# Kernel optimization log

Hardware: AMD Instinct MI355X
Metric: run time of the kernel (lower is better)

The kernel has to match this reference:

```python
import jax, jax.numpy as jnp
import numpy as np

N_NODES = 50000
N_EDGES = 800000
N_GRAPHS = 8
BN_EPS = 1e-5


def setup_inputs() -> dict:
    key = jax.random.key(0)
    ks = iter(jax.random.split(key, 40))
    d = {}
    d["x"] = jax.random.normal(next(ks), (N_NODES, 3), dtype=jnp.float32)
    d["edge_index"] = jax.random.randint(next(ks), (2, N_EDGES), 0, N_NODES, dtype=jnp.int32)
    d["batch"] = jnp.sort(jax.random.randint(next(ks), (N_NODES,), 0, N_GRAPHS, dtype=jnp.int32))
    conv_in = [3, 64, 128]  # dense concat widths feeding each GCN layer
    for i, cin in enumerate(conv_in):
        d[f"W{i}"] = jax.random.normal(next(ks), (cin, 64), dtype=jnp.float32) * (1.0 / np.sqrt(cin))
        d[f"b{i}"] = jax.random.normal(next(ks), (64,), dtype=jnp.float32) * 0.05
        d[f"g{i}"] = jax.random.uniform(next(ks), (64,), dtype=jnp.float32) + 0.5
        d[f"beta{i}"] = jax.random.normal(next(ks), (64,), dtype=jnp.float32) * 0.05
        d[f"rm{i}"] = jax.random.normal(next(ks), (64,), dtype=jnp.float32) * 0.05
        d[f"rv{i}"] = jax.random.uniform(next(ks), (64,), dtype=jnp.float32) + 0.5
    def lin(k, i, o):
        return (jax.random.normal(k, (i, o), dtype=jnp.float32) * (1.0 / np.sqrt(i)),)
    d["enc_w0"], = lin(next(ks), 256, 128); d["enc_b0"] = jax.random.normal(next(ks), (128,), jnp.float32) * 0.05
    d["enc_w1"], = lin(next(ks), 128, 64); d["enc_b1"] = jax.random.normal(next(ks), (64,), jnp.float32) * 0.05
    d["dec_w0"], = lin(next(ks), 64, 32); d["dec_b0"] = jax.random.normal(next(ks), (32,), jnp.float32) * 0.05
    d["dec_w1"], = lin(next(ks), 32, 1); d["dec_b1"] = jax.random.normal(next(ks), (1,), jnp.float32) * 0.05
    return d


def reference(x, edge_index, batch,
              W0, b0, g0, beta0, rm0, rv0,
              W1, b1, g1, beta1, rm1, rv1,
              W2, b2, g2, beta2, rm2, rv2,
              enc_w0, enc_b0, enc_w1, enc_b1,
              dec_w0, dec_b0, dec_w1, dec_b1):
    N = x.shape[0]
    loops = jnp.arange(N, dtype=edge_index.dtype)
    src = jnp.concatenate([edge_index[0], loops])  # GCNConv adds self loops
    dst = jnp.concatenate([edge_index[1], loops])
    deg = jax.ops.segment_sum(jnp.ones_like(src, dtype=x.dtype), dst, num_segments=N)
    dinv = jnp.where(deg > 0, jax.lax.rsqrt(deg), 0.0)
    coef = (dinv[src] * dinv[dst])[:, None]  # symmetric normalization per edge

    def conv_bn_relu(h, W, b, g, beta, rm, rv):
        hw = h @ W                                    # [N, 64]
        out = jax.ops.segment_sum(hw[src] * coef, dst, num_segments=N) + b
        out = (out - rm) * (g * jax.lax.rsqrt(rv + BN_EPS)) + beta  # BN eval mode
        return jax.nn.relu(out)

    params = [(W0, b0, g0, beta0, rm0, rv0),
              (W1, b1, g1, beta1, rm1, rv1),
              (W2, b2, g2, beta2, rm2, rv2)]
    prev = []
    h = x
    for p in params:  # dense connectivity: concat all previous concat-outputs
        h = conv_bn_relu(h, *p)
        h = jnp.concatenate(prev + [h], axis=1)
        prev.append(h)

    e = jax.nn.relu(jax.nn.relu(h @ enc_w0 + enc_b0) @ enc_w1 + enc_b1)  # [N, 64]
    counts = jax.ops.segment_sum(jnp.ones((N,), x.dtype), batch, num_segments=N_GRAPHS)
    gfeat = jax.ops.segment_sum(e, batch, num_segments=N_GRAPHS) / jnp.maximum(counts, 1.0)[:, None]
    out = jax.nn.relu(gfeat @ dec_w0 + dec_b0) @ dec_w1 + dec_b1  # [G, 1]
    return out[:, 0]  # torch.squeeze(output, 1) since num_classes == 1
```

## Files before the change

kernel.cpp:

```cpp
#include <hip/hip_runtime.h>
#include <hip/hip_fp16.h>

#define NN 50000
#define NE 800000
#define NG 8
#define BN_EPS 1e-5f
#define NBLK ((NN + 255) / 256)
#define NPART 8
#define HLD 192

typedef __attribute__((ext_vector_type(8))) short bf16x8;
typedef __attribute__((ext_vector_type(4))) float f32x4;

static __device__ __forceinline__ unsigned short f2bf(float f) {
    unsigned int u = __float_as_uint(f);
    unsigned int r = (u + 0x7FFFu + ((u >> 16) & 1u)) >> 16;
    return (unsigned short)r;
}
static __device__ __forceinline__ float bf2f(unsigned short h) {
    return __uint_as_float((unsigned int)h << 16);
}


__global__ __launch_bounds__(256) void count_deg(const int4* __restrict__ dst4,
                                                 int* __restrict__ degi) {
    int t = blockIdx.x * 256 + threadIdx.x;
    if (t < NE / 4) {
        int4 d = dst4[t];
        atomicAdd(&degi[d.x], 1);
        atomicAdd(&degi[d.y], 1);
        atomicAdd(&degi[d.z], 1);
        atomicAdd(&degi[d.w], 1);
    }
}

__global__ __launch_bounds__(256) void scan_partial(const int* __restrict__ degi,
                                                    const float* __restrict__ x,
                                                    int* __restrict__ rowptr,
                                                    int* __restrict__ bsum,
                                                    float* __restrict__ dinv,
                                                    float* __restrict__ xs) {
    __shared__ int sh[256];
    const int tid = threadIdx.x;
    const int i = blockIdx.x * 256 + tid;
    int v = (i < NN) ? degi[i] : 0;
    if (i < NN) {
        float di = rsqrtf((float)(v + 1));
        dinv[i] = di;
        xs[i * 3 + 0] = x[i * 3 + 0] * di;
        xs[i * 3 + 1] = x[i * 3 + 1] * di;
        xs[i * 3 + 2] = x[i * 3 + 2] * di;
    }
    sh[tid] = v;
    __syncthreads();
#pragma unroll
    for (int off = 1; off < 256; off <<= 1) {
        int t = (tid >= off) ? sh[tid - off] : 0;
        __syncthreads();
        sh[tid] += t;
        __syncthreads();
    }
    if (i < NN) rowptr[i] = sh[tid] - v;
    if (tid == 255) bsum[blockIdx.x] = sh[255];
}

__global__ __launch_bounds__(256) void scan_bsums(int* __restrict__ bsum) {
    __shared__ int sh[256];
    const int tid = threadIdx.x;
    int v = (tid < NBLK) ? bsum[tid] : 0;
    sh[tid] = v;
    __syncthreads();
#pragma unroll
    for (int off = 1; off < 256; off <<= 1) {
        int t = (tid >= off) ? sh[tid - off] : 0;
        __syncthreads();
        sh[tid] += t;
        __syncthreads();
    }
    if (tid < NBLK) bsum[tid] = sh[tid] - v;
}

__global__ __launch_bounds__(256) void scan_finalize(const int* __restrict__ bsum,
                                                     int* __restrict__ rowptr,
                                                     int* __restrict__ cursor) {
    const int i = blockIdx.x * 256 + threadIdx.x;
    if (i < NN) {
        int r = rowptr[i] + bsum[blockIdx.x];
        rowptr[i] = r;
        cursor[i] = r;
    }
    if (i == 0) rowptr[NN] = NE;
}

__global__ __launch_bounds__(256) void fill_csr(const int* __restrict__ src,
                                                const int* __restrict__ dst,
                                                int* __restrict__ cursor,
                                                unsigned short* __restrict__ esrc16) {
    int e = blockIdx.x * 256 + threadIdx.x;
    if (e < NE) {
        int s = src[e], d = dst[e];
        int p = atomicAdd(&cursor[d], 1);
        esrc16[p] = (unsigned short)s;
    }
}


static __device__ __forceinline__ void pack_one(const float* W, int NOUT, int li,
                                                float v_override, bool use_override,
                                                unsigned short* ph, unsigned short* pl) {
    int j = li & 7;
    int lane = (li >> 3) & 63;
    int rest = li >> 9;
    int NF = NOUT >> 4;
    int f = rest % NF, ks = rest / NF;
    int k = ks * 32 + (lane >> 4) * 8 + j;
    int col = f * 16 + (lane & 15);
    float v = use_override ? v_override : W[k * NOUT + col];
    unsigned short hi = f2bf(v);
    ph[li] = hi;
    pl[li] = f2bf(v - bf2f(hi));
}

__global__ __launch_bounds__(256) void pack_all(
        const float* __restrict__ W1, const float* __restrict__ W2,
        const float* __restrict__ We0, const float* __restrict__ We1,
        unsigned short* __restrict__ Wp1h, unsigned short* __restrict__ Wp1l,
        unsigned short* __restrict__ Wp2h, unsigned short* __restrict__ Wp2l,
        unsigned short* __restrict__ We0h, unsigned short* __restrict__ We0l,
        unsigned short* __restrict__ We1h, unsigned short* __restrict__ We1l,
        float* __restrict__ gfeat_part) {
    int idx = blockIdx.x * 256 + threadIdx.x;
    if (idx < NPART * NG * 64) gfeat_part[idx] = 0.0f;
    if (idx < 4096) {
        pack_one(W1, 64, idx, 0.f, false, Wp1h, Wp1l);
    } else if (idx < 12288) {
        pack_one(W2, 64, idx - 4096, 0.f, false, Wp2h, Wp2l);
    } else if (idx < 36864) {
        int li = idx - 12288;
        int j = li & 7;
        int lane = (li >> 3) & 63;
        int rest = li >> 9;
        int f = rest % 8, ks = rest / 8;
        int k = ks * 32 + (lane >> 4) * 8 + j;
        int col = f * 16 + (lane & 15);
        float v = (k < 64) ? (We0[k * 128 + col] + We0[(k + 64) * 128 + col])
                           : We0[(k + 64) * 128 + col];
        pack_one(nullptr, 128, li, v, true, We0h, We0l);
    } else if (idx < 45056) {
        pack_one(We1, 64, idx - 36864, 0.f, false, We1h, We1l);
    }
}


template<int K>
__global__ __launch_bounds__(256, 2) void mfma_tab(
        const unsigned short* __restrict__ Ahi,
        const unsigned short* __restrict__ Alo, int lda,
        const unsigned short* __restrict__ Bph,
        const unsigned short* __restrict__ Bpl,
        const float* __restrict__ dinv,
        __half* __restrict__ outH) {
    constexpr int KS = K / 32;
    const int wave = threadIdx.x >> 6;
    const int lane = threadIdx.x & 63;
    const int rbase = blockIdx.x * 64 + wave * 16;
    int arow = rbase + (lane & 15);
    if (arow >= NN) arow = NN - 1;
    const int kbase = (lane >> 4) * 8;

    bf16x8 bh[KS][4], bl[KS][4];
#pragma unroll
    for (int ks = 0; ks < KS; ks++)
#pragma unroll
        for (int f = 0; f < 4; f++) {
            bh[ks][f] = *reinterpret_cast<const bf16x8*>(Bph + (size_t)((ks * 4 + f) * 64 + lane) * 8);
            bl[ks][f] = *reinterpret_cast<const bf16x8*>(Bpl + (size_t)((ks * 4 + f) * 64 + lane) * 8);
        }

    const unsigned short* pa_hi = Ahi + (size_t)arow * lda + kbase;
    const unsigned short* pa_lo = Alo + (size_t)arow * lda + kbase;
    bf16x8 ah[KS], al[KS];
#pragma unroll
    for (int ks = 0; ks < KS; ks++) {
        ah[ks] = *reinterpret_cast<const bf16x8*>(pa_hi + ks * 32);
        al[ks] = *reinterpret_cast<const bf16x8*>(pa_lo + ks * 32);
    }

    f32x4 acc[4];
#pragma unroll
    for (int f = 0; f < 4; f++) acc[f] = (f32x4){0.f, 0.f, 0.f, 0.f};

#pragma unroll
    for (int ks = 0; ks < KS; ks++)
#pragma unroll
        for (int f = 0; f < 4; f++) {
            acc[f] = __builtin_amdgcn_mfma_f32_16x16x32_bf16(ah[ks], bh[ks][f], acc[f], 0, 0, 0);
            acc[f] = __builtin_amdgcn_mfma_f32_16x16x32_bf16(ah[ks], bl[ks][f], acc[f], 0, 0, 0);
            acc[f] = __builtin_amdgcn_mfma_f32_16x16x32_bf16(al[ks], bh[ks][f], acc[f], 0, 0, 0);
        }

    const int drow0 = rbase + (lane >> 4) * 4;
    const int dcol = lane & 15;
#pragma unroll
    for (int f = 0; f < 4; f++) {
#pragma unroll
        for (int r = 0; r < 4; r++) {
            int row = drow0 + r;
            if (row < NN)
                outH[(size_t)row * 64 + f * 16 + dcol] = __float2half(acc[f][r] * dinv[row]);
        }
    }
}


__global__ __launch_bounds__(256, 2) void enc_fused(
        const unsigned short* __restrict__ Hhi,
        const unsigned short* __restrict__ Hlo,
        const unsigned short* __restrict__ We0h, const unsigned short* __restrict__ We0l,
        const float* __restrict__ b0,
        const unsigned short* __restrict__ We1h, const unsigned short* __restrict__ We1l,
        const float* __restrict__ b1,
        const int* __restrict__ batch,
        float* __restrict__ gfeat_part) {
    __shared__ float ldsT[4][16][133];
    __shared__ float poolw[4][64];
    __shared__ float pool[NG][64];
    const int tid = threadIdx.x;
    const int wave = tid >> 6;
    const int lane = tid & 63;
    const int rbase = blockIdx.x * 64 + wave * 16;

    int arow = rbase + (lane & 15);
    if (arow >= NN) arow = NN - 1;
    const int kbase = (lane >> 4) * 8;
    f32x4 acc[8];
#pragma unroll
    for (int f = 0; f < 8; f++) acc[f] = (f32x4){0.f, 0.f, 0.f, 0.f};

    const unsigned short* pa_hi = Hhi + (size_t)arow * HLD + kbase;
    const unsigned short* pa_lo = Hlo + (size_t)arow * HLD + kbase;

    bf16x8 cbh[8], cbl[8], nbh[8], nbl[8];
#pragma unroll
    for (int f = 0; f < 8; f++) {
        cbh[f] = *reinterpret_cast<const bf16x8*>(We0h + (size_t)(f * 64 + lane) * 8);
        cbl[f] = *reinterpret_cast<const bf16x8*>(We0l + (size_t)(f * 64 + lane) * 8);
    }
#pragma unroll
    for (int ks = 0; ks < 6; ks++) {
        if (ks < 5) {
#pragma unroll
            for (int f = 0; f < 8; f++) {
                nbh[f] = *reinterpret_cast<const bf16x8*>(We0h + (size_t)(((ks + 1) * 8 + f) * 64 + lane) * 8);
                nbl[f] = *reinterpret_cast<const bf16x8*>(We0l + (size_t)(((ks + 1) * 8 + f) * 64 + lane) * 8);
            }
        }
        bf16x8 ah = *reinterpret_cast<const bf16x8*>(pa_hi + ks * 32);
        bf16x8 al = *reinterpret_cast<const bf16x8*>(pa_lo + ks * 32);
#pragma unroll
        for (int f = 0; f < 8; f++) {
            acc[f] = __builtin_amdgcn_mfma_f32_16x16x32_bf16(ah, cbh[f], acc[f], 0, 0, 0);
            acc[f] = __builtin_amdgcn_mfma_f32_16x16x32_bf16(ah, cbl[f], acc[f], 0, 0, 0);
            acc[f] = __builtin_amdgcn_mfma_f32_16x16x32_bf16(al, cbh[f], acc[f], 0, 0, 0);
        }
        if (ks < 5) {
#pragma unroll
            for (int f = 0; f < 8; f++) { cbh[f] = nbh[f]; cbl[f] = nbl[f]; }
        }
    }

    const int lrow0 = (lane >> 4) * 4;
    const int dcol = lane & 15;
#pragma unroll
    for (int f = 0; f < 8; f++) {
#pragma unroll
        for (int r = 0; r < 4; r++) {
            float v = fmaxf(acc[f][r] + b0[f * 16 + dcol], 0.0f);
            ldsT[wave][lrow0 + r][f * 16 + dcol] = v;
        }
    }
    __syncthreads();

    bf16x8 wbh[4][4], wbl[4][4];
#pragma unroll
    for (int ks = 0; ks < 4; ks++)
#pragma unroll
        for (int f = 0; f < 4; f++) {
            wbh[ks][f] = *reinterpret_cast<const bf16x8*>(We1h + (size_t)((ks * 4 + f) * 64 + lane) * 8);
            wbl[ks][f] = *reinterpret_cast<const bf16x8*>(We1l + (size_t)((ks * 4 + f) * 64 + lane) * 8);
        }

    f32x4 acc2[4];
#pragma unroll
    for (int f = 0; f < 4; f++) acc2[f] = (f32x4){0.f, 0.f, 0.f, 0.f};

    const int trow = lane & 15;
#pragma unroll
    for (int ks = 0; ks < 4; ks++) {
        bf16x8 ah, al;
#pragma unroll
        for (int j = 0; j < 8; j++) {
            float tv = ldsT[wave][trow][ks * 32 + (lane >> 4) * 8 + j];
            unsigned short hi = f2bf(tv);
            ah[j] = (short)hi;
            al[j] = (short)f2bf(tv - bf2f(hi));
        }
#pragma unroll
        for (int f = 0; f < 4; f++) {
            acc2[f] = __builtin_amdgcn_mfma_f32_16x16x32_bf16(ah, wbh[ks][f], acc2[f], 0, 0, 0);
            acc2[f] = __builtin_amdgcn_mfma_f32_16x16x32_bf16(ah, wbl[ks][f], acc2[f], 0, 0, 0);
            acc2[f] = __builtin_amdgcn_mfma_f32_16x16x32_bf16(al, wbh[ks][f], acc2[f], 0, 0, 0);
        }
    }

    float vout[4][4];
#pragma unroll
    for (int f = 0; f < 4; f++)
#pragma unroll
        for (int r = 0; r < 4; r++) {
            int row = rbase + lrow0 + r;
            vout[f][r] = (row < NN) ? fmaxf(acc2[f][r] + b1[f * 16 + dcol], 0.0f) : 0.0f;
        }

    const int blk_row0 = blockIdx.x * 64;
    const int blk_rowN = min(blk_row0 + 63, NN - 1);
    const int g0 = batch[blk_row0];
    const int p = blockIdx.x & (NPART - 1);

    if (g0 == batch[blk_rowN]) {
#pragma unroll
        for (int f = 0; f < 4; f++) {
            float s = (vout[f][0] + vout[f][1]) + (vout[f][2] + vout[f][3]);
            s += __shfl_xor(s, 16, 64);
            s += __shfl_xor(s, 32, 64);
            if ((lane >> 4) == 0) poolw[wave][f * 16 + dcol] = s;
        }
        __syncthreads();
        if (tid < 64) {
            float s = (poolw[0][tid] + poolw[1][tid]) + (poolw[2][tid] + poolw[3][tid]);
            atomicAdd(&gfeat_part[(p * NG + g0) * 64 + tid], s);
        }
    } else {
        for (int i = tid; i < NG * 64; i += 256) ((float*)pool)[i] = 0.0f;
        __syncthreads();
#pragma unroll
        for (int r = 0; r < 4; r++) {
            int row = rbase + lrow0 + r;
            if (row < NN) {
                int g = batch[row];
#pragma unroll
                for (int f = 0; f < 4; f++)
                    atomicAdd(&pool[g][f * 16 + dcol], vout[f][r]);
            }
        }
        __syncthreads();
        for (int i = tid; i < NG * 64; i += 256) {
            float s = ((float*)pool)[i];
            if (s != 0.0f) atomicAdd(&gfeat_part[p * NG * 64 + i], s);
        }
    }
}


__global__ __launch_bounds__(256) void agg_x3(
        const float* __restrict__ xs,
        const int* __restrict__ rowptr,
        const unsigned short* __restrict__ esrc16,
        const float* __restrict__ dinv,
        float* __restrict__ ax) {
    const int i = blockIdx.x * 256 + threadIdx.x;
    if (i >= NN) return;
    float a0 = xs[i * 3 + 0];
    float a1 = xs[i * 3 + 1];
    float a2 = xs[i * 3 + 2];
    const int beg = rowptr[i], end = rowptr[i + 1];
    int e = beg;
    for (; e + 3 < end; e += 4) {
        int s0 = esrc16[e], s1 = esrc16[e + 1], s2 = esrc16[e + 2], s3 = esrc16[e + 3];
        a0 += xs[s0 * 3 + 0] + xs[s1 * 3 + 0] + xs[s2 * 3 + 0] + xs[s3 * 3 + 0];
        a1 += xs[s0 * 3 + 1] + xs[s1 * 3 + 1] + xs[s2 * 3 + 1] + xs[s3 * 3 + 1];
        a2 += xs[s0 * 3 + 2] + xs[s1 * 3 + 2] + xs[s2 * 3 + 2] + xs[s3 * 3 + 2];
    }
    for (; e < end; e++) {
        int s = esrc16[e];
        a0 += xs[s * 3 + 0];
        a1 += xs[s * 3 + 1];
        a2 += xs[s * 3 + 2];
    }
    const float di = dinv[i];
    ax[i * 3 + 0] = a0 * di;
    ax[i * 3 + 1] = a1 * di;
    ax[i * 3 + 2] = a2 * di;
}


__global__ __launch_bounds__(256) void l0_bn_relu(
        const float* __restrict__ ax, const float* __restrict__ W0,
        const float* __restrict__ b, const float* __restrict__ g,
        const float* __restrict__ beta, const float* __restrict__ rm,
        const float* __restrict__ rv,
        unsigned short* __restrict__ Hhi, unsigned short* __restrict__ Hlo) {
    const int t = blockIdx.x * 256 + threadIdx.x;
    const int row = t >> 6;
    const int ch = t & 63;
    if (row >= NN) return;
    float a0 = ax[row * 3 + 0], a1 = ax[row * 3 + 1], a2 = ax[row * 3 + 2];
    float v = a0 * W0[0 * 64 + ch] + a1 * W0[1 * 64 + ch] + a2 * W0[2 * 64 + ch] + b[ch];
    float sc = g[ch] * rsqrtf(rv[ch] + BN_EPS);
    v = (v - rm[ch]) * sc + beta[ch];
    v = fmaxf(v, 0.0f);
    unsigned short hi = f2bf(v);
    Hhi[(size_t)row * HLD + ch] = hi;
    Hlo[(size_t)row * HLD + ch] = f2bf(v - bf2f(hi));
}


__global__ __launch_bounds__(256) void gather_bn_relu(
        const __half2* __restrict__ tab2,
        const int* __restrict__ rowptr,
        const unsigned short* __restrict__ esrc16,
        const float* __restrict__ dinv,
        const float* __restrict__ b, const float* __restrict__ g,
        const float* __restrict__ beta, const float* __restrict__ rm,
        const float* __restrict__ rv,
        unsigned short* __restrict__ Hhi, unsigned short* __restrict__ Hlo, int cbase) {
    const int wid = (blockIdx.x * 256 + threadIdx.x) >> 6;
    const int lane = threadIdx.x & 63;
    const int c2 = lane & 31;
    const int grp = lane >> 5;
    if (wid >= NN) return;
    const int beg = rowptr[wid], end = rowptr[wid + 1];
    float a0 = 0.0f, a1 = 0.0f;
    int e = beg + grp;
    for (; e + 14 < end; e += 16) {
        int s0 = esrc16[e],      s1 = esrc16[e + 2],  s2 = esrc16[e + 4],  s3 = esrc16[e + 6];
        int s4 = esrc16[e + 8],  s5 = esrc16[e + 10], s6 = esrc16[e + 12], s7 = esrc16[e + 14];
        float2 f0 = __half22float2(tab2[(size_t)s0 * 32 + c2]);
        float2 f1 = __half22float2(tab2[(size_t)s1 * 32 + c2]);
        float2 f2 = __half22float2(tab2[(size_t)s2 * 32 + c2]);
        float2 f3 = __half22float2(tab2[(size_t)s3 * 32 + c2]);
        float2 f4 = __half22float2(tab2[(size_t)s4 * 32 + c2]);
        float2 f5 = __half22float2(tab2[(size_t)s5 * 32 + c2]);
        float2 f6 = __half22float2(tab2[(size_t)s6 * 32 + c2]);
        float2 f7 = __half22float2(tab2[(size_t)s7 * 32 + c2]);
        a0 += ((f0.x + f1.x) + (f2.x + f3.x)) + ((f4.x + f5.x) + (f6.x + f7.x));
        a1 += ((f0.y + f1.y) + (f2.y + f3.y)) + ((f4.y + f5.y) + (f6.y + f7.y));
    }
    for (; e + 6 < end; e += 8) {
        int s0 = esrc16[e], s1 = esrc16[e + 2], s2 = esrc16[e + 4], s3 = esrc16[e + 6];
        float2 f0 = __half22float2(tab2[(size_t)s0 * 32 + c2]);
        float2 f1 = __half22float2(tab2[(size_t)s1 * 32 + c2]);
        float2 f2 = __half22float2(tab2[(size_t)s2 * 32 + c2]);
        float2 f3 = __half22float2(tab2[(size_t)s3 * 32 + c2]);
        a0 += (f0.x + f1.x) + (f2.x + f3.x);
        a1 += (f0.y + f1.y) + (f2.y + f3.y);
    }
    for (; e < end; e += 2) {
        float2 f = __half22float2(tab2[(size_t)esrc16[e] * 32 + c2]);
        a0 += f.x;
        a1 += f.y;
    }
    a0 += __shfl_xor(a0, 32, 64);
    a1 += __shfl_xor(a1, 32, 64);
    float2 fs = __half22float2(tab2[(size_t)wid * 32 + c2]);
    a0 += fs.x;
    a1 += fs.y;
    const float di = dinv[wid];
    a0 *= di;
    a1 *= di;
    const int ch0 = 2 * c2, ch1 = 2 * c2 + 1;
    float v0 = (a0 + b[ch0] - rm[ch0]) * (g[ch0] * rsqrtf(rv[ch0] + BN_EPS)) + beta[ch0];
    float v1 = (a1 + b[ch1] - rm[ch1]) * (g[ch1] * rsqrtf(rv[ch1] + BN_EPS)) + beta[ch1];
    v0 = fmaxf(v0, 0.0f);
    v1 = fmaxf(v1, 0.0f);
    if (grp == 0) {
        unsigned short h0 = f2bf(v0), h1 = f2bf(v1);
        unsigned short l0 = f2bf(v0 - bf2f(h0)), l1 = f2bf(v1 - bf2f(h1));
        size_t o = (size_t)wid * HLD + cbase + ch0;
        *reinterpret_cast<unsigned int*>(&Hhi[o]) = (unsigned int)h0 | ((unsigned int)h1 << 16);
        *reinterpret_cast<unsigned int*>(&Hlo[o]) = (unsigned int)l0 | ((unsigned int)l1 << 16);
    }
}


__global__ __launch_bounds__(256) void dec_kernel(
        const float* __restrict__ gfeat_part, const int* __restrict__ batch,
        const float* __restrict__ w0, const float* __restrict__ b0,
        const float* __restrict__ w1, const float* __restrict__ b1,
        float* __restrict__ out) {
    __shared__ float mg[NG][64];
    __shared__ float mc[NG];
    __shared__ float t1[NG][32];
    const int tid = threadIdx.x;
    for (int idx = tid; idx < NG * 64; idx += 256) {
        float s = 0.0f;
#pragma unroll
        for (int p = 0; p < NPART; p++) s += gfeat_part[p * NG * 64 + idx];
        mg[idx >> 6][idx & 63] = s;
    }
    if (tid < NG) {
        int lo = 0, hi = NN;
        while (lo < hi) { int m = (lo + hi) >> 1; if (batch[m] < tid) lo = m + 1; else hi = m; }
        int s0 = lo;
        lo = 0; hi = NN;
        while (lo < hi) { int m = (lo + hi) >> 1; if (batch[m] < tid + 1) lo = m + 1; else hi = m; }
        mc[tid] = (float)(lo - s0);
    }
    __syncthreads();
    const int g = tid >> 5, c = tid & 31;
    float inv = 1.0f / fmaxf(mc[g], 1.0f);
    float acc = b0[c];
    for (int k = 0; k < 64; k++)
        acc = fmaf(mg[g][k] * inv, w0[k * 32 + c], acc);
    t1[g][c] = fmaxf(acc, 0.0f);
    __syncthreads();
    if (tid < NG) {
        float o = b1[0];
        for (int c2 = 0; c2 < 32; c2++) o = fmaf(t1[tid][c2], w1[c2], o);
        out[tid] = o;
    }
}


extern "C" void kernel_launch(void* const* d_in, const int* in_sizes, int n_in,
                              void* d_out, int out_size, void* d_ws, size_t ws_size,
                              hipStream_t stream) {
    const float* x      = (const float*)d_in[0];
    const int*   ei     = (const int*)d_in[1];
    const int*   batch  = (const int*)d_in[2];
    const float* W0     = (const float*)d_in[3];
    const float* b0     = (const float*)d_in[4];
    const float* g0     = (const float*)d_in[5];
    const float* beta0  = (const float*)d_in[6];
    const float* rm0    = (const float*)d_in[7];
    const float* rv0    = (const float*)d_in[8];
    const float* W1     = (const float*)d_in[9];
    const float* b1     = (const float*)d_in[10];
    const float* g1     = (const float*)d_in[11];
    const float* beta1  = (const float*)d_in[12];
    const float* rm1    = (const float*)d_in[13];
    const float* rv1    = (const float*)d_in[14];
    const float* W2     = (const float*)d_in[15];
    const float* b2     = (const float*)d_in[16];
    const float* g2     = (const float*)d_in[17];
    const float* beta2  = (const float*)d_in[18];
    const float* rm2    = (const float*)d_in[19];
    const float* rv2    = (const float*)d_in[20];
    const float* enc_w0 = (const float*)d_in[21];
    const float* enc_b0 = (const float*)d_in[22];
    const float* enc_w1 = (const float*)d_in[23];
    const float* enc_b1 = (const float*)d_in[24];
    const float* dec_w0 = (const float*)d_in[25];
    const float* dec_b0 = (const float*)d_in[26];
    const float* dec_w1 = (const float*)d_in[27];
    const float* dec_b1 = (const float*)d_in[28];

    const int* esrc = ei;
    const int* edst = ei + NE;

    char* wsb = (char*)d_ws;
    unsigned short* Hhi = (unsigned short*)wsb;
    unsigned short* Hlo = Hhi + (size_t)NN * HLD;
    int*   degi   = (int*)(Hlo + (size_t)NN * HLD);
    int*   rowptr = degi + NN;
    int*   cursor = rowptr + NN + 1;
    unsigned short* esrc16 = (unsigned short*)(cursor + NN);
    __half* tabh  = (__half*)(esrc16 + NE);
    float* dinv   = (float*)(tabh + (size_t)NN * 64);
    float* xs     = dinv + NN;
    float* ax     = xs + (size_t)NN * 3;
    float* gfeat_part = ax + (size_t)NN * 3;
    int*   bsum   = (int*)(gfeat_part + NPART * NG * 64);
    unsigned short* wp = (unsigned short*)(bsum + NBLK);
    unsigned short* Wp1h = wp;              unsigned short* Wp1l = Wp1h + 64 * 64;
    unsigned short* Wp2h = Wp1l + 64 * 64;  unsigned short* Wp2l = Wp2h + 128 * 64;
    unsigned short* We0h = Wp2l + 128 * 64; unsigned short* We0l = We0h + 192 * 128;
    unsigned short* We1h = We0l + 192 * 128;unsigned short* We1l = We1h + 128 * 64;

    hipMemsetAsync(degi, 0, NN * sizeof(int), stream);

    count_deg<<<(NE / 4 + 255) / 256, 256, 0, stream>>>((const int4*)edst, degi);
    scan_partial<<<NBLK, 256, 0, stream>>>(degi, x, rowptr, bsum, dinv, xs);
    scan_bsums<<<1, 256, 0, stream>>>(bsum);
    scan_finalize<<<NBLK, 256, 0, stream>>>(bsum, rowptr, cursor);
    fill_csr<<<(NE + 255) / 256, 256, 0, stream>>>(esrc, edst, cursor, esrc16);

    pack_all<<<(45056 + 255) / 256, 256, 0, stream>>>(W1, W2, enc_w0, enc_w1,
                                                      Wp1h, Wp1l, Wp2h, Wp2l,
                                                      We0h, We0l, We1h, We1l, gfeat_part);

    const int GRID_MFMA = (NN + 63) / 64;
    const int GRID_64   = (NN * 64 + 255) / 256;

    agg_x3<<<NBLK, 256, 0, stream>>>(xs, rowptr, esrc16, dinv, ax);
    l0_bn_relu<<<GRID_64, 256, 0, stream>>>(ax, W0, b0, g0, beta0, rm0, rv0, Hhi, Hlo);

    mfma_tab<64><<<GRID_MFMA, 256, 0, stream>>>(Hhi, Hlo, HLD, Wp1h, Wp1l, dinv, tabh);
    gather_bn_relu<<<GRID_64, 256, 0, stream>>>((const __half2*)tabh, rowptr, esrc16, dinv,
                                                b1, g1, beta1, rm1, rv1, Hhi, Hlo, 64);

    mfma_tab<128><<<GRID_MFMA, 256, 0, stream>>>(Hhi, Hlo, HLD, Wp2h, Wp2l, dinv, tabh);
    gather_bn_relu<<<GRID_64, 256, 0, stream>>>((const __half2*)tabh, rowptr, esrc16, dinv,
                                                b2, g2, beta2, rm2, rv2, Hhi, Hlo, 128);

    enc_fused<<<GRID_MFMA, 256, 0, stream>>>(Hhi, Hlo, We0h, We0l, enc_b0,
                                             We1h, We1l, enc_b1, batch, gfeat_part);

    dec_kernel<<<1, 256, 0, stream>>>(gfeat_part, batch, dec_w0, dec_b0, dec_w1, dec_b1, (float*)d_out);
}
```

Baseline: 235.8 us.

## Fuse layer-0 aggregation with BN/ReLU and trim preprocessing launches

Replaces the separate agg_x3 and l0_bn_relu kernels with one agg_l0 kernel. It assigns one wave per node: lanes gather neighbour features, reduce with shuffles, then each lane computes one output channel. This removes the intermediate ax buffer. The degree memset moves into pack_all, which now runs first. The block-sum scan is folded into scan_finalize, where every block redoes the small scan over block sums. Together these cut several kernel launches and a global round-trip, in exchange for idle lanes in the wave-per-node gather on low-degree nodes and redundant scan work per block.

```diff
diff --git a/kernel.cpp b/kernel.cpp
--- a/kernel.cpp
+++ b/kernel.cpp
@@ -19,89 +19,6 @@
 }
 static __device__ __forceinline__ float bf2f(unsigned short h) {
     return __uint_as_float((unsigned int)h << 16);
-}
-
-
-__global__ __launch_bounds__(256) void count_deg(const int4* __restrict__ dst4,
-                                                 int* __restrict__ degi) {
-    int t = blockIdx.x * 256 + threadIdx.x;
-    if (t < NE / 4) {
-        int4 d = dst4[t];
-        atomicAdd(&degi[d.x], 1);
-        atomicAdd(&degi[d.y], 1);
-        atomicAdd(&degi[d.z], 1);
-        atomicAdd(&degi[d.w], 1);
-    }
-}
-
-__global__ __launch_bounds__(256) void scan_partial(const int* __restrict__ degi,
-                                                    const float* __restrict__ x,
-                                                    int* __restrict__ rowptr,
-                                                    int* __restrict__ bsum,
-                                                    float* __restrict__ dinv,
-                                                    float* __restrict__ xs) {
-    __shared__ int sh[256];
-    const int tid = threadIdx.x;
-    const int i = blockIdx.x * 256 + tid;
-    int v = (i < NN) ? degi[i] : 0;
-    if (i < NN) {
-        float di = rsqrtf((float)(v + 1));
-        dinv[i] = di;
-        xs[i * 3 + 0] = x[i * 3 + 0] * di;
-        xs[i * 3 + 1] = x[i * 3 + 1] * di;
-        xs[i * 3 + 2] = x[i * 3 + 2] * di;
-    }
-    sh[tid] = v;
-    __syncthreads();
-#pragma unroll
-    for (int off = 1; off < 256; off <<= 1) {
-        int t = (tid >= off) ? sh[tid - off] : 0;
-        __syncthreads();
-        sh[tid] += t;
-        __syncthreads();
-    }
-    if (i < NN) rowptr[i] = sh[tid] - v;
-    if (tid == 255) bsum[blockIdx.x] = sh[255];
-}
-
-__global__ __launch_bounds__(256) void scan_bsums(int* __restrict__ bsum) {
-    __shared__ int sh[256];
-    const int tid = threadIdx.x;
-    int v = (tid < NBLK) ? bsum[tid] : 0;
-    sh[tid] = v;
-    __syncthreads();
-#pragma unroll
-    for (int off = 1; off < 256; off <<= 1) {
-        int t = (tid >= off) ? sh[tid - off] : 0;
-        __syncthreads();
-        sh[tid] += t;
-        __syncthreads();
-    }
-    if (tid < NBLK) bsum[tid] = sh[tid] - v;
-}
-
-__global__ __launch_bounds__(256) void scan_finalize(const int* __restrict__ bsum,
-                                                     int* __restrict__ rowptr,
-                                                     int* __restrict__ cursor) {
-    const int i = blockIdx.x * 256 + threadIdx.x;
-    if (i < NN) {
-        int r = rowptr[i] + bsum[blockIdx.x];
-        rowptr[i] = r;
-        cursor[i] = r;
-    }
-    if (i == 0) rowptr[NN] = NE;
-}
-
-__global__ __launch_bounds__(256) void fill_csr(const int* __restrict__ src,
-                                                const int* __restrict__ dst,
-                                                int* __restrict__ cursor,
-                                                unsigned short* __restrict__ esrc16) {
-    int e = blockIdx.x * 256 + threadIdx.x;
-    if (e < NE) {
-        int s = src[e], d = dst[e];
-        int p = atomicAdd(&cursor[d], 1);
-        esrc16[p] = (unsigned short)s;
-    }
 }
 
 
@@ -128,8 +45,9 @@
         unsigned short* __restrict__ Wp2h, unsigned short* __restrict__ Wp2l,
         unsigned short* __restrict__ We0h, unsigned short* __restrict__ We0l,
         unsigned short* __restrict__ We1h, unsigned short* __restrict__ We1l,
-        float* __restrict__ gfeat_part) {
+        int* __restrict__ degi, float* __restrict__ gfeat_part) {
     int idx = blockIdx.x * 256 + threadIdx.x;
+    if (idx < NN) degi[idx] = 0;
     if (idx < NPART * NG * 64) gfeat_part[idx] = 0.0f;
     if (idx < 4096) {
         pack_one(W1, 64, idx, 0.f, false, Wp1h, Wp1l);
@@ -152,6 +70,128 @@
 }
 
 
+__global__ __launch_bounds__(256) void count_deg(const int4* __restrict__ dst4,
+                                                 int* __restrict__ degi) {
+    int t = blockIdx.x * 256 + threadIdx.x;
+    if (t < NE / 4) {
+        int4 d = dst4[t];
+        atomicAdd(&degi[d.x], 1);
+        atomicAdd(&degi[d.y], 1);
+        atomicAdd(&degi[d.z], 1);
+        atomicAdd(&degi[d.w], 1);
+    }
+}
+
+__global__ __launch_bounds__(256) void scan_partial(const int* __restrict__ degi,
+                                                    const float* __restrict__ x,
+                                                    int* __restrict__ rowptr,
+                                                    int* __restrict__ bsum,
+                                                    float* __restrict__ dinv,
+                                                    float* __restrict__ xs) {
+    __shared__ int sh[256];
+    const int tid = threadIdx.x;
+    const int i = blockIdx.x * 256 + tid;
+    int v = (i < NN) ? degi[i] : 0;
+    if (i < NN) {
+        float di = rsqrtf((float)(v + 1));
+        dinv[i] = di;
+        xs[i * 3 + 0] = x[i * 3 + 0] * di;
+        xs[i * 3 + 1] = x[i * 3 + 1] * di;
+        xs[i * 3 + 2] = x[i * 3 + 2] * di;
+    }
+    sh[tid] = v;
+    __syncthreads();
+#pragma unroll
+    for (int off = 1; off < 256; off <<= 1) {
+        int t = (tid >= off) ? sh[tid - off] : 0;
+        __syncthreads();
+        sh[tid] += t;
+        __syncthreads();
+    }
+    if (i < NN) rowptr[i] = sh[tid] - v;
+    if (tid == 255) bsum[blockIdx.x] = sh[255];
+}
+
+__global__ __launch_bounds__(256) void scan_finalize(const int* __restrict__ bsum,
+                                                     int* __restrict__ rowptr,
+                                                     int* __restrict__ cursor) {
+    __shared__ int sh[256];
+    const int tid = threadIdx.x;
+    int v = (tid < NBLK) ? bsum[tid] : 0;
+    sh[tid] = v;
+    __syncthreads();
+#pragma unroll
+    for (int off = 1; off < 256; off <<= 1) {
+        int t = (tid >= off) ? sh[tid - off] : 0;
+        __syncthreads();
+        sh[tid] += t;
+        __syncthreads();
+    }
+    const int base = (blockIdx.x == 0) ? 0 : sh[blockIdx.x - 1];
+    const int i = blockIdx.x * 256 + tid;
+    if (i < NN) {
+        int r = rowptr[i] + base;
+        rowptr[i] = r;
+        cursor[i] = r;
+    }
+    if (i == 0) rowptr[NN] = NE;
+}
+
+__global__ __launch_bounds__(256) void fill_csr(const int* __restrict__ src,
+                                                const int* __restrict__ dst,
+                                                int* __restrict__ cursor,
+                                                unsigned short* __restrict__ esrc16) {
+    int e = blockIdx.x * 256 + threadIdx.x;
+    if (e < NE) {
+        int s = src[e], d = dst[e];
+        int p = atomicAdd(&cursor[d], 1);
+        esrc16[p] = (unsigned short)s;
+    }
+}
+
+
+__global__ __launch_bounds__(256) void agg_l0(
+        const float* __restrict__ xs,
+        const int* __restrict__ rowptr,
+        const unsigned short* __restrict__ esrc16,
+        const float* __restrict__ dinv,
+        const float* __restrict__ W0, const float* __restrict__ b,
+        const float* __restrict__ g, const float* __restrict__ beta,
+        const float* __restrict__ rm, const float* __restrict__ rv,
+        unsigned short* __restrict__ Hhi, unsigned short* __restrict__ Hlo) {
+    const int wid = (blockIdx.x * 256 + threadIdx.x) >> 6;
+    const int lane = threadIdx.x & 63;
+    if (wid >= NN) return;
+    const int beg = rowptr[wid], end = rowptr[wid + 1];
+    float a0 = 0.0f, a1 = 0.0f, a2 = 0.0f;
+    for (int e = beg + lane; e < end; e += 64) {
+        int s = esrc16[e];
+        a0 += xs[s * 3 + 0];
+        a1 += xs[s * 3 + 1];
+        a2 += xs[s * 3 + 2];
+    }
+#pragma unroll
+    for (int off = 32; off >= 1; off >>= 1) {
+        a0 += __shfl_xor(a0, off, 64);
+        a1 += __shfl_xor(a1, off, 64);
+        a2 += __shfl_xor(a2, off, 64);
+    }
+    a0 += xs[wid * 3 + 0];
+    a1 += xs[wid * 3 + 1];
+    a2 += xs[wid * 3 + 2];
+    const float di = dinv[wid];
+    a0 *= di; a1 *= di; a2 *= di;
+    const int ch = lane;
+    float v = a0 * W0[ch] + a1 * W0[64 + ch] + a2 * W0[128 + ch] + b[ch];
+    float sc = g[ch] * rsqrtf(rv[ch] + BN_EPS);
+    v = (v - rm[ch]) * sc + beta[ch];
+    v = fmaxf(v, 0.0f);
+    unsigned short hi = f2bf(v);
+    Hhi[(size_t)wid * HLD + ch] = hi;
+    Hlo[(size_t)wid * HLD + ch] = f2bf(v - bf2f(hi));
+}
+
+
 template<int K>
 __global__ __launch_bounds__(256, 2) void mfma_tab(
         const unsigned short* __restrict__ Ahi,
@@ -359,59 +399,6 @@
             if (s != 0.0f) atomicAdd(&gfeat_part[p * NG * 64 + i], s);
         }
     }
-}
-
-
-__global__ __launch_bounds__(256) void agg_x3(
-        const float* __restrict__ xs,
-        const int* __restrict__ rowptr,
-        const unsigned short* __restrict__ esrc16,
-        const float* __restrict__ dinv,
-        float* __restrict__ ax) {
-    const int i = blockIdx.x * 256 + threadIdx.x;
-    if (i >= NN) return;
-    float a0 = xs[i * 3 + 0];
-    float a1 = xs[i * 3 + 1];
-    float a2 = xs[i * 3 + 2];
-    const int beg = rowptr[i], end = rowptr[i + 1];
-    int e = beg;
-    for (; e + 3 < end; e += 4) {
-        int s0 = esrc16[e], s1 = esrc16[e + 1], s2 = esrc16[e + 2], s3 = esrc16[e + 3];
-        a0 += xs[s0 * 3 + 0] + xs[s1 * 3 + 0] + xs[s2 * 3 + 0] + xs[s3 * 3 + 0];
-        a1 += xs[s0 * 3 + 1] + xs[s1 * 3 + 1] + xs[s2 * 3 + 1] + xs[s3 * 3 + 1];
-        a2 += xs[s0 * 3 + 2] + xs[s1 * 3 + 2] + xs[s2 * 3 + 2] + xs[s3 * 3 + 2];
-    }
-    for (; e < end; e++) {
-        int s = esrc16[e];
-        a0 += xs[s * 3 + 0];
-        a1 += xs[s * 3 + 1];
-        a2 += xs[s * 3 + 2];
-    }
-    const float di = dinv[i];
-    ax[i * 3 + 0] = a0 * di;
-    ax[i * 3 + 1] = a1 * di;
-    ax[i * 3 + 2] = a2 * di;
-}
-
-
-__global__ __launch_bounds__(256) void l0_bn_relu(
-        const float* __restrict__ ax, const float* __restrict__ W0,
-        const float* __restrict__ b, const float* __restrict__ g,
-        const float* __restrict__ beta, const float* __restrict__ rm,
-        const float* __restrict__ rv,
-        unsigned short* __restrict__ Hhi, unsigned short* __restrict__ Hlo) {
-    const int t = blockIdx.x * 256 + threadIdx.x;
-    const int row = t >> 6;
-    const int ch = t & 63;
-    if (row >= NN) return;
-    float a0 = ax[row * 3 + 0], a1 = ax[row * 3 + 1], a2 = ax[row * 3 + 2];
-    float v = a0 * W0[0 * 64 + ch] + a1 * W0[1 * 64 + ch] + a2 * W0[2 * 64 + ch] + b[ch];
-    float sc = g[ch] * rsqrtf(rv[ch] + BN_EPS);
-    v = (v - rm[ch]) * sc + beta[ch];
-    v = fmaxf(v, 0.0f);
-    unsigned short hi = f2bf(v);
-    Hhi[(size_t)row * HLD + ch] = hi;
-    Hlo[(size_t)row * HLD + ch] = f2bf(v - bf2f(hi));
 }
 
 
@@ -568,8 +555,7 @@
     __half* tabh  = (__half*)(esrc16 + NE);
     float* dinv   = (float*)(tabh + (size_t)NN * 64);
     float* xs     = dinv + NN;
-    float* ax     = xs + (size_t)NN * 3;
-    float* gfeat_part = ax + (size_t)NN * 3;
+    float* gfeat_part = xs + (size_t)NN * 3;
     int*   bsum   = (int*)(gfeat_part + NPART * NG * 64);
     unsigned short* wp = (unsigned short*)(bsum + NBLK);
     unsigned short* Wp1h = wp;              unsigned short* Wp1l = Wp1h + 64 * 64;
@@ -577,23 +563,20 @@
     unsigned short* We0h = Wp2l + 128 * 64; unsigned short* We0l = We0h + 192 * 128;
     unsigned short* We1h = We0l + 192 * 128;unsigned short* We1l = We1h + 128 * 64;
 
-    hipMemsetAsync(degi, 0, NN * sizeof(int), stream);
+    const int GRID_MFMA = (NN + 63) / 64;
+    const int GRID_64   = (NN * 64 + 255) / 256;
+
+    pack_all<<<NBLK, 256, 0, stream>>>(W1, W2, enc_w0, enc_w1,
+                                       Wp1h, Wp1l, Wp2h, Wp2l,
+                                       We0h, We0l, We1h, We1l, degi, gfeat_part);
 
     count_deg<<<(NE / 4 + 255) / 256, 256, 0, stream>>>((const int4*)edst, degi);
     scan_partial<<<NBLK, 256, 0, stream>>>(degi, x, rowptr, bsum, dinv, xs);
-    scan_bsums<<<1, 256, 0, stream>>>(bsum);
     scan_finalize<<<NBLK, 256, 0, stream>>>(bsum, rowptr, cursor);
     fill_csr<<<(NE + 255) / 256, 256, 0, stream>>>(esrc, edst, cursor, esrc16);
 
-    pack_all<<<(45056 + 255) / 256, 256, 0, stream>>>(W1, W2, enc_w0, enc_w1,
-                                                      Wp1h, Wp1l, Wp2h, Wp2l,
-                                                      We0h, We0l, We1h, We1l, gfeat_part);
-
-    const int GRID_MFMA = (NN + 63) / 64;
-    const int GRID_64   = (NN * 64 + 255) / 256;
-
-    agg_x3<<<NBLK, 256, 0, stream>>>(xs, rowptr, esrc16, dinv, ax);
-    l0_bn_relu<<<GRID_64, 256, 0, stream>>>(ax, W0, b0, g0, beta0, rm0, rv0, Hhi, Hlo);
+    agg_l0<<<GRID_64, 256, 0, stream>>>(xs, rowptr, esrc16, dinv,
+                                        W0, b0, g0, beta0, rm0, rv0, Hhi, Hlo);
 
     mfma_tab<64><<<GRID_MFMA, 256, 0, stream>>>(Hhi, Hlo, HLD, Wp1h, Wp1l, dinv, tabh);
     gather_bn_relu<<<GRID_64, 256, 0, stream>>>((const __half2*)tabh, rowptr, esrc16, dinv,
```

Measured after the change: 230.5 us. 1.02x faster.
